# Optimization experiments

Measured on AMD Instinct MI355X. Metric: run time of the kernel, lower is better.

## Reference

```python
import jax, jax.numpy as jnp
import numpy as np

K = 9  # kernel_size (kNN neighbors, includes self since loop=True)


def _knn_edges(x_f, batch, k):
    # x_f: [N, C]. Full pairwise squared distances, masked across batch groups.
    N = x_f.shape[0]
    sq = jnp.sum(x_f * x_f, axis=1)
    d2 = sq[:, None] - 2.0 * (x_f @ x_f.T) + sq[None, :]          # [N, N]
    same = batch[:, None] == batch[None, :]
    d2 = jnp.where(same, d2, jnp.inf)
    neg_d, idx = jax.lax.top_k(-d2, k)                             # k nearest per query row
    valid = jnp.isfinite(neg_d)                                    # guard tiny groups (<k nodes)
    src = idx.reshape(-1)                                          # neighbor -> source
    tgt = jnp.repeat(jnp.arange(N), k)                             # query    -> target
    return src, tgt, valid.reshape(-1)


def _cheb_conv(x_f, src, tgt, valid, W0, W1, bias):
    # ChebConv, K=2, normalization='sym', lambda_max=2.0:
    #   out = x @ W0 + (L_hat x) @ W1 + b,  L_hat = -D^{-1/2} A D^{-1/2} (diag 0)
    N = x_f.shape[0]
    w = jnp.where(valid & (src != tgt), 1.0, 0.0)                  # remove_self_loops
    deg = jax.ops.segment_sum(w, src, num_segments=N)
    dis = jnp.where(deg > 0, jax.lax.rsqrt(jnp.maximum(deg, 1e-30)), 0.0)
    norm = -dis[src] * w * dis[tgt]                                # off-diag of scaled Laplacian
    Tx1 = jax.ops.segment_sum(norm[:, None] * x_f[src], tgt, num_segments=N)
    return x_f @ W0 + Tx1 @ W1 + bias


def setup_inputs() -> dict:
    key = jax.random.key(0)
    k1, k2, k3, k4 = jax.random.split(key, 4)
    B, C, H, W = 8, 192, 32, 32
    Cout = 192
    return {
        "x": jax.random.normal(k1, (B, C, H, W), dtype=jnp.float32),
        "W0": jax.random.normal(k2, (C, Cout), dtype=jnp.float32) * (1.0 / np.sqrt(C)),
        "W1": jax.random.normal(k3, (C, Cout), dtype=jnp.float32) * (1.0 / np.sqrt(C)),
        "bias": jax.random.normal(k4, (Cout,), dtype=jnp.float32) * 0.01,
    }


def reference(x, W0, W1, bias):
    B, C, H, W = x.shape
    N = B * H * W
    x_f = jnp.transpose(x, (0, 2, 3, 1)).reshape(N, C)             # flat_nodes: [B*H*W, C]
    # torch.linspace(0, B, steps=N, dtype=int64) -> truncated float linspace
    batch = jnp.linspace(0.0, float(B), N).astype(jnp.int32)
    src, tgt, valid = _knn_edges(x_f, batch, K)
    return _cheb_conv(x_f, src, tgt, valid, W0, W1, bias)
```

## Files before the change

### kernel.cpp

```cpp
#include <hip/hip_runtime.h>
#include <math.h>

#define NN 8192
#define CF 192
#define KNN 9
#define NSPL 8
#define PKS 12

typedef __bf16 v8bf __attribute__((ext_vector_type(8)));
typedef float f32x16 __attribute__((ext_vector_type(16)));
typedef float f32x4 __attribute__((ext_vector_type(4)));

__device__ __forceinline__ int group_start(int g) {
    int s = (8191 * g + 7) >> 3;
    return s > 8192 ? 8192 : s;
}

__device__ __forceinline__ float disf(int d) {
    return d > 0 ? 1.0f / sqrtf((float)d) : 0.0f;
}

__device__ __forceinline__ unsigned short f2bf(float f) {
    unsigned u = __float_as_uint(f);
    unsigned r = (u + 0x7FFFu + ((u >> 16) & 1u)) >> 16;
    return (unsigned short)r;
}
__device__ __forceinline__ float bf2f(unsigned short h) {
    return __uint_as_float(((unsigned)h) << 16);
}

__global__ __launch_bounds__(256) void transpose_kernel(
    const float* __restrict__ x, unsigned short* __restrict__ xh,
    unsigned short* __restrict__ xl, float* __restrict__ sq,
    int* __restrict__ deg)
{
    __shared__ float tile[32][65];
    int b = blockIdx.x, ht = blockIdx.y;
    int hw0 = ht * 64;
    int tid = threadIdx.x;
    if (tid < 64) deg[(b * 16 + ht) * 64 + tid] = 0;

    float sacc[8];
#pragma unroll
    for (int p = 0; p < 8; ++p) sacc[p] = 0.0f;

    for (int ct = 0; ct < 6; ++ct) {
        int c0 = ct * 32;
        __syncthreads();
#pragma unroll
        for (int p = 0; p < 8; ++p) {
            int c  = p * 4 + (tid >> 6);
            int hw = tid & 63;
            tile[c][hw] = x[(size_t)b * 196608 + (size_t)(c0 + c) * 1024 + hw0 + hw];
        }
        __syncthreads();
#pragma unroll
        for (int p = 0; p < 8; ++p) {
            int hw = p * 8 + (tid >> 5);
            int cc = tid & 31;
            float v = tile[cc][hw];
            size_t o = (size_t)(b * 1024 + hw0 + hw) * CF + c0 + cc;
            unsigned short h = f2bf(v);
            xh[o] = h;
            xl[o] = f2bf(v - bf2f(h));
            sacc[p] = fmaf(v, v, sacc[p]);
        }
    }
#pragma unroll
    for (int p = 0; p < 8; ++p) {
        float s = sacc[p];
#pragma unroll
        for (int off = 16; off > 0; off >>= 1) s += __shfl_xor(s, off, 32);
        if ((tid & 31) == 0)
            sq[(size_t)(b * 1024 + hw0 + p * 8 + (tid >> 5))] = s;
    }
}

__global__ __launch_bounds__(256, 2) void knn_kernel(
    const unsigned short* __restrict__ xh, const unsigned short* __restrict__ xl,
    const float* __restrict__ sq,
    float* __restrict__ pk_d, int* __restrict__ pk_i)
{
    int bid = blockIdx.x;
    int g = bid >> 7;
    int rem = bid & 127;
    int qb = rem >> 3;
    int split = rem & 7;
    int gs = group_start(g);
    int gsize = group_start(g + 1) - gs;
    int q0 = qb * 64;
    int nq = gsize - q0; if (nq > 64) nq = 64;
    if (nq <= 0) return;
    int c0 = split * 128;
    int ncc = gsize - c0; if (ncc > 128) ncc = 128;

    int tid = threadIdx.x;

    if (ncc <= 0) {
        if (tid < nq) {
            int q = gs + q0 + tid;
            size_t base = ((size_t)q * NSPL + split) * PKS;
#pragma unroll
            for (int j = 0; j < KNN; ++j) { pk_d[base + j] = __builtin_inff(); pk_i[base + j] = -1; }
        }
        return;
    }

    __shared__ __align__(16) char smem[28192];
    unsigned short (*Ah)[24] = (unsigned short(*)[24])smem;
    unsigned short (*Al)[24] = (unsigned short(*)[24])(smem + 3072);
    unsigned short (*Bh)[24] = (unsigned short(*)[24])(smem + 6144);
    unsigned short (*Bl)[24] = (unsigned short(*)[24])(smem + 12288);
    float (*ld)[KNN][65] = (float(*)[KNN][65])smem;
    int   (*li)[KNN][65] = (int(*)[KNN][65])(smem + 9360);
    float (*Ds)[37] = (float(*)[37])(smem + 18720);
    __shared__ float sqc_s[128];
    __shared__ float sqq_s[64];

    int lane = tid & 63, w = tid >> 6;
    int arow = (w & 1) * 32 + (lane & 31);
    int k8 = (lane >> 5) * 8;
    int brow0 = (w >> 1) * 64 + (lane & 31);

    if (tid < 64) {
        int qo = q0 + tid; if (qo > gsize - 1) qo = gsize - 1;
        sqq_s[tid] = sq[gs + qo];
    }
    if (tid < 128) {
        sqc_s[tid] = (tid < 128 && tid < ncc) ? sq[gs + c0 + tid] : __builtin_inff();
    }

    int a_hl = tid >> 7, a_r = (tid >> 1) & 63, a_half = tid & 1;
    int a_qo = q0 + a_r; if (a_qo > gsize - 1) a_qo = gsize - 1;
    const unsigned short* a_src = (a_hl ? xl : xh)
        + (size_t)(gs + a_qo) * CF + a_half * 8;
    unsigned short* a_dst = (a_hl ? (unsigned short*)Al : (unsigned short*)Ah)
        + a_r * 24 + a_half * 8;

    int b_r = (tid >> 1) & 127, b_half = tid & 1;
    int b_co = c0 + b_r; if (b_co > gsize - 1) b_co = gsize - 1;
    const unsigned short* b_src0 = xh + (size_t)(gs + b_co) * CF + b_half * 8;
    const unsigned short* b_src1 = xl + (size_t)(gs + b_co) * CF + b_half * 8;
    unsigned short* b_dst0 = (unsigned short*)Bh + b_r * 24 + b_half * 8;
    unsigned short* b_dst1 = (unsigned short*)Bl + b_r * 24 + b_half * 8;

    f32x16 acc[2];
#pragma unroll
    for (int t = 0; t < 2; ++t)
#pragma unroll
        for (int r = 0; r < 16; ++r) acc[t][r] = 0.0f;

    uint4 rA  = *(const uint4*)a_src;
    uint4 rB0 = *(const uint4*)b_src0;
    uint4 rB1 = *(const uint4*)b_src1;

    for (int kb = 0; kb < 12; ++kb) {
        __syncthreads();
        *(uint4*)a_dst  = rA;
        *(uint4*)b_dst0 = rB0;
        *(uint4*)b_dst1 = rB1;
        __syncthreads();
        if (kb < 11) {
            rA  = *(const uint4*)(a_src  + (kb + 1) * 16);
            rB0 = *(const uint4*)(b_src0 + (kb + 1) * 16);
            rB1 = *(const uint4*)(b_src1 + (kb + 1) * 16);
        }
        v8bf a_hi = *(const v8bf*)&Ah[arow][k8];
        v8bf a_lo = *(const v8bf*)&Al[arow][k8];
#pragma unroll
        for (int t = 0; t < 2; ++t) {
            v8bf b_hi = *(const v8bf*)&Bh[brow0 + t * 32][k8];
            v8bf b_lo = *(const v8bf*)&Bl[brow0 + t * 32][k8];
            acc[t] = __builtin_amdgcn_mfma_f32_32x32x16_bf16(a_hi, b_hi, acc[t], 0, 0, 0);
            acc[t] = __builtin_amdgcn_mfma_f32_32x32x16_bf16(a_lo, b_hi, acc[t], 0, 0, 0);
            acc[t] = __builtin_amdgcn_mfma_f32_32x32x16_bf16(a_hi, b_lo, acc[t], 0, 0, 0);
        }
    }

    int sq_ = tid & 63, sch = tid >> 6;
    float sqqv = sqq_s[sq_];
    float pd[KNN]; int pi[KNN];
#pragma unroll
    for (int j = 0; j < KNN; ++j) { pd[j] = __builtin_inff(); pi[j] = -1; }

#pragma unroll
    for (int qt = 0; qt < 4; ++qt) {
        __syncthreads();
        if ((w >> 1) == (qt >> 1)) {
#pragma unroll
            for (int r = 0; r < 16; ++r) {
                int row = (w & 1) * 32 + (r & 3) + 8 * (r >> 2) + 4 * (lane >> 5);
                Ds[row][lane & 31] = acc[qt & 1][r];
            }
        }
        __syncthreads();
        float dv[8], cv[8];
#pragma unroll
        for (int j8 = 0; j8 < 8; ++j8) {
            dv[j8] = Ds[sq_][sch * 8 + j8];
            cv[j8] = sqc_s[qt * 32 + sch * 8 + j8];
        }
#pragma unroll
        for (int j8 = 0; j8 < 8; ++j8) {
            float d = (sqqv - 2.0f * dv[j8]) + cv[j8];
            if (d < pd[KNN - 1]) {
                pd[KNN - 1] = d; pi[KNN - 1] = gs + c0 + qt * 32 + sch * 8 + j8;
#pragma unroll
                for (int j = KNN - 1; j > 0; --j) {
                    if (pd[j] < pd[j - 1]) {
                        float tf = pd[j]; pd[j] = pd[j - 1]; pd[j - 1] = tf;
                        int tn = pi[j]; pi[j] = pi[j - 1]; pi[j - 1] = tn;
                    }
                }
            }
        }
    }

#pragma unroll
    for (int j = 0; j < KNN; ++j) { ld[sch][j][sq_] = pd[j]; li[sch][j][sq_] = pi[j]; }
    __syncthreads();

    if (tid < 64) {
        float dL[4][KNN]; int iL[4][KNN];
#pragma unroll
        for (int ch = 0; ch < 4; ++ch)
#pragma unroll
            for (int j = 0; j < KNN; ++j) {
                dL[ch][j] = ld[ch][j][tid];
                iL[ch][j] = li[ch][j][tid];
            }
        float td[KNN]; int ti[KNN];
#pragma unroll
        for (int j = 0; j < KNN; ++j) { td[j] = __builtin_inff(); ti[j] = -1; }
#pragma unroll
        for (int ch = 0; ch < 4; ++ch) {
#pragma unroll
            for (int j0 = 0; j0 < KNN; ++j0) {
                float d = dL[ch][j0];
                if (!(d < td[KNN - 1])) break;
                td[KNN - 1] = d; ti[KNN - 1] = iL[ch][j0];
#pragma unroll
                for (int j = KNN - 1; j > 0; --j) {
                    if (td[j] < td[j - 1]) {
                        float tf = td[j]; td[j] = td[j - 1]; td[j - 1] = tf;
                        int tn = ti[j]; ti[j] = ti[j - 1]; ti[j - 1] = tn;
                    }
                }
            }
        }
        if (tid < nq) {
            int q = gs + q0 + tid;
            size_t base = ((size_t)q * NSPL + split) * PKS;
#pragma unroll
            for (int j = 0; j < KNN; ++j) { pk_d[base + j] = td[j]; pk_i[base + j] = ti[j]; }
        }
    }
}

__global__ __launch_bounds__(64) void merge_kernel(
    const float* __restrict__ pk_d, const int* __restrict__ pk_i,
    int* __restrict__ edges, int* __restrict__ deg,
    const float* __restrict__ W0, const float* __restrict__ W1,
    unsigned short* __restrict__ wt)
{
    __shared__ float wtile[32][33];
    int tid = threadIdx.x;
    if (blockIdx.x >= 128) {
        int wid = blockIdx.x - 128;
        int mat = wid / 36, rem2 = wid % 36;
        int k0 = (rem2 / 6) * 32, n0 = (rem2 % 6) * 32;
        const float* W = mat ? W1 : W0;
#pragma unroll
        for (int p = 0; p < 4; ++p) {
            int idx = p * 64 + tid;
            int k = idx >> 3, n4 = (idx & 7) * 4;
            *(float4*)&wtile[k][n4] =
                *(const float4*)(W + (size_t)(k0 + k) * CF + n0 + n4);
        }
        __syncthreads();
#pragma unroll
        for (int p = 0; p < 4; ++p) {
            int idx = p * 64 + tid;
            int n = idx >> 3, k4 = (idx & 7) * 4;
            ushort4 h;
            h.x = f2bf(wtile[k4 + 0][n]); h.y = f2bf(wtile[k4 + 1][n]);
            h.z = f2bf(wtile[k4 + 2][n]); h.w = f2bf(wtile[k4 + 3][n]);
            *(ushort4*)(wt + (size_t)mat * 36864 + (size_t)(n0 + n) * CF + k0 + k4) = h;
        }
        return;
    }
    int q = blockIdx.x * 64 + tid;
    float td[KNN]; int ti[KNN];
#pragma unroll
    for (int j = 0; j < KNN; ++j) { td[j] = __builtin_inff(); ti[j] = -1; }
#pragma unroll
    for (int sb = 0; sb < 2; ++sb) {
        float sd[4][KNN]; int si[4][KNN];
#pragma unroll
        for (int s2 = 0; s2 < 4; ++s2) {
            int s = sb * 4 + s2;
            const float* pd = pk_d + ((size_t)q * NSPL + s) * PKS;
            const int*   pp = pk_i + ((size_t)q * NSPL + s) * PKS;
            float4 d0 = *(const float4*)pd;
            float4 d1 = *(const float4*)(pd + 4);
            sd[s2][0] = d0.x; sd[s2][1] = d0.y; sd[s2][2] = d0.z; sd[s2][3] = d0.w;
            sd[s2][4] = d1.x; sd[s2][5] = d1.y; sd[s2][6] = d1.z; sd[s2][7] = d1.w;
            sd[s2][8] = pd[8];
            int4 i0 = *(const int4*)pp;
            int4 i1 = *(const int4*)(pp + 4);
            si[s2][0] = i0.x; si[s2][1] = i0.y; si[s2][2] = i0.z; si[s2][3] = i0.w;
            si[s2][4] = i1.x; si[s2][5] = i1.y; si[s2][6] = i1.z; si[s2][7] = i1.w;
            si[s2][8] = pp[8];
        }
#pragma unroll
        for (int s2 = 0; s2 < 4; ++s2) {
#pragma unroll
            for (int j0 = 0; j0 < KNN; ++j0) {
                float d = sd[s2][j0];
                if (!(d < td[KNN - 1])) break;
                td[KNN - 1] = d; ti[KNN - 1] = si[s2][j0];
#pragma unroll
                for (int j = KNN - 1; j > 0; --j) {
                    if (td[j] < td[j - 1]) {
                        float tf = td[j]; td[j] = td[j - 1]; td[j - 1] = tf;
                        int tn = ti[j]; ti[j] = ti[j - 1]; ti[j - 1] = tn;
                    }
                }
            }
        }
    }
#pragma unroll
    for (int j = 0; j < KNN; ++j) {
        int id = ti[j];
        edges[q * KNN + j] = id;
        if (id >= 0 && id != q) atomicAdd(&deg[id], 1);
    }
}

__global__ __launch_bounds__(256, 2) void out_kernel(
    const unsigned short* __restrict__ xh, const unsigned short* __restrict__ wt,
    const int* __restrict__ edges, const int* __restrict__ deg,
    const float* __restrict__ bias, float* __restrict__ out)
{
    __shared__ __align__(16) unsigned short A0s[16][200];
    __shared__ __align__(16) unsigned short A1s[16][200];
    __shared__ unsigned short Wts[2][CF][32];
    __shared__ float coef_s[16][KNN];
    __shared__ int   nb_s[16][KNN];

    int r0 = blockIdx.x * 16;
    int tid = threadIdx.x;

    for (int t = tid; t < 384; t += 256) {
        int i = t / 24, c8 = (t % 24) * 8;
        *(uint4*)&A0s[i][c8] = *(const uint4*)(xh + (size_t)(r0 + i) * CF + c8);
    }
    if (tid < 16 * KNN) {
        int i = tid / KNN, j = tid % KNN;
        int q = r0 + i;
        int id = edges[q * KNN + j];
        float cf = 0.0f; int s = q;
        if (id >= 0 && id != q) { cf = -disf(deg[id]) * disf(deg[q]); s = id; }
        coef_s[i][j] = cf; nb_s[i][j] = s;
    }
    __syncthreads();
    for (int e = tid; e < 16 * CF / 8; e += 256) {
        int i = e / 24, c8 = (e % 24) * 8;
        float a[8];
#pragma unroll
        for (int j = 0; j < 8; ++j) a[j] = 0.0f;
#pragma unroll
        for (int t = 0; t < KNN; ++t) {
            float cf = coef_s[i][t];
            uint4 v = *(const uint4*)(xh + (size_t)nb_s[i][t] * CF + c8);
            const unsigned short* pv = (const unsigned short*)&v;
#pragma unroll
            for (int j = 0; j < 8; ++j) a[j] = fmaf(cf, bf2f(pv[j]), a[j]);
        }
        uint4 hv;
        hv.x = (unsigned)f2bf(a[0]) | ((unsigned)f2bf(a[1]) << 16);
        hv.y = (unsigned)f2bf(a[2]) | ((unsigned)f2bf(a[3]) << 16);
        hv.z = (unsigned)f2bf(a[4]) | ((unsigned)f2bf(a[5]) << 16);
        hv.w = (unsigned)f2bf(a[6]) | ((unsigned)f2bf(a[7]) << 16);
        *(uint4*)&A1s[i][c8] = hv;
    }

    int lane = tid & 63, w = tid >> 6;
    int m = lane & 15;
    int kq = (lane >> 4) * 8;
    f32x4 acc[3];
#pragma unroll
    for (int t = 0; t < 3; ++t)
#pragma unroll
        for (int r = 0; r < 4; ++r) acc[t][r] = 0.0f;

    for (int kt = 0; kt < 6; ++kt) {
        __syncthreads();
#pragma unroll
        for (int p = 0; p < 6; ++p) {
            int f = p * 256 + tid;
            int mat = f / 768, n = (f % 768) / 4, k16 = (f % 4) * 8;
            *(uint4*)&Wts[mat][n][k16] =
                *(const uint4*)(wt + (size_t)mat * 36864 + (size_t)n * CF + kt * 32 + k16);
        }
        __syncthreads();
        v8bf a0 = *(const v8bf*)&A0s[m][kt * 32 + kq];
        v8bf a1 = *(const v8bf*)&A1s[m][kt * 32 + kq];
#pragma unroll
        for (int t3 = 0; t3 < 3; ++t3) {
            int n0 = w * 48 + t3 * 16;
            v8bf w0 = *(const v8bf*)&Wts[0][n0 + m][kq];
            v8bf w1 = *(const v8bf*)&Wts[1][n0 + m][kq];
            acc[t3] = __builtin_amdgcn_mfma_f32_16x16x32_bf16(a0, w0, acc[t3], 0, 0, 0);
            acc[t3] = __builtin_amdgcn_mfma_f32_16x16x32_bf16(a1, w1, acc[t3], 0, 0, 0);
        }
    }

    int col = lane & 15, rb = (lane >> 4) * 4;
#pragma unroll
    for (int t3 = 0; t3 < 3; ++t3) {
        int n0 = w * 48 + t3 * 16;
        float bv = bias[n0 + col];
#pragma unroll
        for (int r = 0; r < 4; ++r)
            out[(size_t)(r0 + rb + r) * CF + n0 + col] = acc[t3][r] + bv;
    }
}

extern "C" void kernel_launch(void* const* d_in, const int* in_sizes, int n_in,
                              void* d_out, int out_size, void* d_ws, size_t ws_size,
                              hipStream_t stream)
{
    const float* x    = (const float*)d_in[0];
    const float* W0   = (const float*)d_in[1];
    const float* W1   = (const float*)d_in[2];
    const float* bias = (const float*)d_in[3];
    float* out = (float*)d_out;

    char* ws = (char*)d_ws;
    unsigned short* xh = (unsigned short*)ws; ws += (size_t)NN * CF * 2;
    unsigned short* xl = (unsigned short*)ws; ws += (size_t)NN * CF * 2;
    float* sq    = (float*)ws;  ws += (size_t)NN * 4;
    int*   deg   = (int*)ws;    ws += (size_t)NN * 4;
    int*   edges = (int*)ws;    ws += (size_t)NN * KNN * 4;

    unsigned short* wt = xl;

    float* pk_d = out;
    int*   pk_i = (int*)(out + (size_t)NN * NSPL * PKS);

    hipLaunchKernelGGL(transpose_kernel, dim3(8, 16), dim3(256), 0, stream,
                       x, xh, xl, sq, deg);
    hipLaunchKernelGGL(knn_kernel, dim3(1152), dim3(256), 0, stream,
                       xh, xl, sq, pk_d, pk_i);
    hipLaunchKernelGGL(merge_kernel, dim3(200), dim3(64), 0, stream,
                       pk_d, pk_i, edges, deg, W0, W1, wt);
    hipLaunchKernelGGL(out_kernel, dim3(512), dim3(256), 0, stream,
                       xh, wt, edges, deg, bias, out);
}
```

Measured before the change: 131.5 us.

## Double-buffer LDS tiles in kNN distance and output GEMM kernels

The kNN distance kernel now double-buffers its A/B bf16 tiles in shared memory with a two-deep register prefetch, so each k-step needs one barrier instead of two. After the GEMM it writes the whole 64x128 distance tile to LDS at once instead of in four barrier-separated quarter passes. The output kernel double-buffers the weight tiles and prefetches them during the neighbor aggregation. The cost is more LDS and more registers per thread, which could reduce occupancy.

```diff
diff --git a/kernel.cpp b/kernel.cpp
--- a/kernel.cpp
+++ b/kernel.cpp
@@ -106,14 +106,8 @@
         return;
     }
 
-    __shared__ __align__(16) char smem[28192];
-    unsigned short (*Ah)[24] = (unsigned short(*)[24])smem;
-    unsigned short (*Al)[24] = (unsigned short(*)[24])(smem + 3072);
-    unsigned short (*Bh)[24] = (unsigned short(*)[24])(smem + 6144);
-    unsigned short (*Bl)[24] = (unsigned short(*)[24])(smem + 12288);
-    float (*ld)[KNN][65] = (float(*)[KNN][65])smem;
-    int   (*li)[KNN][65] = (int(*)[KNN][65])(smem + 9360);
-    float (*Ds)[37] = (float(*)[37])(smem + 18720);
+    __shared__ __align__(16) char smem[36864];
+    unsigned short* sm = (unsigned short*)smem;
     __shared__ float sqc_s[128];
     __shared__ float sqq_s[64];
 
@@ -127,22 +121,21 @@
         sqq_s[tid] = sq[gs + qo];
     }
     if (tid < 128) {
-        sqc_s[tid] = (tid < 128 && tid < ncc) ? sq[gs + c0 + tid] : __builtin_inff();
+        sqc_s[tid] = (tid < ncc) ? sq[gs + c0 + tid] : __builtin_inff();
     }
 
     int a_hl = tid >> 7, a_r = (tid >> 1) & 63, a_half = tid & 1;
     int a_qo = q0 + a_r; if (a_qo > gsize - 1) a_qo = gsize - 1;
     const unsigned short* a_src = (a_hl ? xl : xh)
         + (size_t)(gs + a_qo) * CF + a_half * 8;
-    unsigned short* a_dst = (a_hl ? (unsigned short*)Al : (unsigned short*)Ah)
-        + a_r * 24 + a_half * 8;
+    int a_off = a_hl * 1536 + a_r * 24 + a_half * 8;
 
     int b_r = (tid >> 1) & 127, b_half = tid & 1;
     int b_co = c0 + b_r; if (b_co > gsize - 1) b_co = gsize - 1;
     const unsigned short* b_src0 = xh + (size_t)(gs + b_co) * CF + b_half * 8;
     const unsigned short* b_src1 = xl + (size_t)(gs + b_co) * CF + b_half * 8;
-    unsigned short* b_dst0 = (unsigned short*)Bh + b_r * 24 + b_half * 8;
-    unsigned short* b_dst1 = (unsigned short*)Bl + b_r * 24 + b_half * 8;
+    int b_off0 = 3072 + b_r * 24 + b_half * 8;
+    int b_off1 = 6144 + b_r * 24 + b_half * 8;
 
     f32x16 acc[2];
 #pragma unroll
@@ -150,61 +143,77 @@
 #pragma unroll
         for (int r = 0; r < 16; ++r) acc[t][r] = 0.0f;
 
-    uint4 rA  = *(const uint4*)a_src;
-    uint4 rB0 = *(const uint4*)b_src0;
-    uint4 rB1 = *(const uint4*)b_src1;
-
+    uint4 sA[2], sB0[2], sB1[2];
+    sA[0]  = *(const uint4*)(a_src);       sA[1]  = *(const uint4*)(a_src + 16);
+    sB0[0] = *(const uint4*)(b_src0);      sB0[1] = *(const uint4*)(b_src0 + 16);
+    sB1[0] = *(const uint4*)(b_src1);      sB1[1] = *(const uint4*)(b_src1 + 16);
+    *(uint4*)(sm + a_off)  = sA[0];
+    *(uint4*)(sm + b_off0) = sB0[0];
+    *(uint4*)(sm + b_off1) = sB1[0];
+    sA[0]  = *(const uint4*)(a_src  + 32);
+    sB0[0] = *(const uint4*)(b_src0 + 32);
+    sB1[0] = *(const uint4*)(b_src1 + 32);
+    __syncthreads();
+
+#pragma unroll
     for (int kb = 0; kb < 12; ++kb) {
-        __syncthreads();
-        *(uint4*)a_dst  = rA;
-        *(uint4*)b_dst0 = rB0;
-        *(uint4*)b_dst1 = rB1;
-        __syncthreads();
+        const int cur = kb & 1, nxt = cur ^ 1;
         if (kb < 11) {
-            rA  = *(const uint4*)(a_src  + (kb + 1) * 16);
-            rB0 = *(const uint4*)(b_src0 + (kb + 1) * 16);
-            rB1 = *(const uint4*)(b_src1 + (kb + 1) * 16);
-        }
-        v8bf a_hi = *(const v8bf*)&Ah[arow][k8];
-        v8bf a_lo = *(const v8bf*)&Al[arow][k8];
+            *(uint4*)(sm + nxt * 9216 + a_off)  = sA[nxt];
+            *(uint4*)(sm + nxt * 9216 + b_off0) = sB0[nxt];
+            *(uint4*)(sm + nxt * 9216 + b_off1) = sB1[nxt];
+        }
+        if (kb < 9) {
+            sA[nxt]  = *(const uint4*)(a_src  + (kb + 3) * 16);
+            sB0[nxt] = *(const uint4*)(b_src0 + (kb + 3) * 16);
+            sB1[nxt] = *(const uint4*)(b_src1 + (kb + 3) * 16);
+        }
+        v8bf a_hi = *(const v8bf*)(sm + cur * 9216 + arow * 24 + k8);
+        v8bf a_lo = *(const v8bf*)(sm + cur * 9216 + 1536 + arow * 24 + k8);
 #pragma unroll
         for (int t = 0; t < 2; ++t) {
-            v8bf b_hi = *(const v8bf*)&Bh[brow0 + t * 32][k8];
-            v8bf b_lo = *(const v8bf*)&Bl[brow0 + t * 32][k8];
+            v8bf b_hi = *(const v8bf*)(sm + cur * 9216 + 3072 + (brow0 + t * 32) * 24 + k8);
+            v8bf b_lo = *(const v8bf*)(sm + cur * 9216 + 6144 + (brow0 + t * 32) * 24 + k8);
             acc[t] = __builtin_amdgcn_mfma_f32_32x32x16_bf16(a_hi, b_hi, acc[t], 0, 0, 0);
             acc[t] = __builtin_amdgcn_mfma_f32_32x32x16_bf16(a_lo, b_hi, acc[t], 0, 0, 0);
             acc[t] = __builtin_amdgcn_mfma_f32_32x32x16_bf16(a_hi, b_lo, acc[t], 0, 0, 0);
         }
-    }
+        __syncthreads();
+    }
+
+    float (*Ds)[133] = (float(*)[133])smem;
+#pragma unroll
+    for (int t = 0; t < 2; ++t)
+#pragma unroll
+        for (int r = 0; r < 16; ++r) {
+            int row = (w & 1) * 32 + (r & 3) + 8 * (r >> 2) + 4 * (lane >> 5);
+            int col = (w >> 1) * 64 + t * 32 + (lane & 31);
+            Ds[row][col] = acc[t][r];
+        }
+    __syncthreads();
 
     int sq_ = tid & 63, sch = tid >> 6;
     float sqqv = sqq_s[sq_];
+    float dv[32], cvv[32];
+#pragma unroll
+    for (int qt = 0; qt < 4; ++qt)
+#pragma unroll
+        for (int j8 = 0; j8 < 8; ++j8) {
+            int c = qt * 32 + sch * 8 + j8;
+            dv[qt * 8 + j8] = Ds[sq_][c];
+            cvv[qt * 8 + j8] = sqc_s[c];
+        }
     float pd[KNN]; int pi[KNN];
 #pragma unroll
     for (int j = 0; j < KNN; ++j) { pd[j] = __builtin_inff(); pi[j] = -1; }
-
-#pragma unroll
-    for (int qt = 0; qt < 4; ++qt) {
-        __syncthreads();
-        if ((w >> 1) == (qt >> 1)) {
-#pragma unroll
-            for (int r = 0; r < 16; ++r) {
-                int row = (w & 1) * 32 + (r & 3) + 8 * (r >> 2) + 4 * (lane >> 5);
-                Ds[row][lane & 31] = acc[qt & 1][r];
-            }
-        }
-        __syncthreads();
-        float dv[8], cv[8];
+#pragma unroll
+    for (int qt = 0; qt < 4; ++qt)
 #pragma unroll
         for (int j8 = 0; j8 < 8; ++j8) {
-            dv[j8] = Ds[sq_][sch * 8 + j8];
-            cv[j8] = sqc_s[qt * 32 + sch * 8 + j8];
-        }
-#pragma unroll
-        for (int j8 = 0; j8 < 8; ++j8) {
-            float d = (sqqv - 2.0f * dv[j8]) + cv[j8];
+            int c = qt * 32 + sch * 8 + j8;
+            float d = (sqqv - 2.0f * dv[qt * 8 + j8]) + cvv[qt * 8 + j8];
             if (d < pd[KNN - 1]) {
-                pd[KNN - 1] = d; pi[KNN - 1] = gs + c0 + qt * 32 + sch * 8 + j8;
+                pd[KNN - 1] = d; pi[KNN - 1] = gs + c0 + c;
 #pragma unroll
                 for (int j = KNN - 1; j > 0; --j) {
                     if (pd[j] < pd[j - 1]) {
@@ -214,8 +223,10 @@
                 }
             }
         }
-    }
-
+    __syncthreads();
+
+    float (*ld)[KNN][65] = (float(*)[KNN][65])smem;
+    int   (*li)[KNN][65] = (int(*)[KNN][65])(smem + 9360);
 #pragma unroll
     for (int j = 0; j < KNN; ++j) { ld[sch][j][sq_] = pd[j]; li[sch][j][sq_] = pi[j]; }
     __syncthreads();
@@ -344,12 +355,31 @@
 {
     __shared__ __align__(16) unsigned short A0s[16][200];
     __shared__ __align__(16) unsigned short A1s[16][200];
-    __shared__ unsigned short Wts[2][CF][32];
+    __shared__ unsigned short Wts[2][2][CF][32];
     __shared__ float coef_s[16][KNN];
     __shared__ int   nb_s[16][KNN];
 
     int r0 = blockIdx.x * 16;
     int tid = threadIdx.x;
+
+#define LDW(dst, kt_)                                                          \
+    _Pragma("unroll")                                                          \
+    for (int p = 0; p < 6; ++p) {                                              \
+        int f = p * 256 + tid;                                                 \
+        int mat = f / 768, n = (f % 768) / 4, k16 = (f % 4) * 8;               \
+        dst[p] = *(const uint4*)(wt + (size_t)mat * 36864 + (size_t)n * CF     \
+                                 + (kt_) * 32 + k16);                          \
+    }
+#define STW(buf_, src)                                                         \
+    _Pragma("unroll")                                                          \
+    for (int p = 0; p < 6; ++p) {                                              \
+        int f = p * 256 + tid;                                                 \
+        int mat = f / 768, n = (f % 768) / 4, k16 = (f % 4) * 8;               \
+        *(uint4*)&Wts[buf_][mat][n][k16] = src[p];                             \
+    }
+
+    uint4 wr[2][6];
+    LDW(wr[0], 0);
 
     for (int t = tid; t < 384; t += 256) {
         int i = t / 24, c8 = (t % 24) * 8;
@@ -363,6 +393,7 @@
         if (id >= 0 && id != q) { cf = -disf(deg[id]) * disf(deg[q]); s = id; }
         coef_s[i][j] = cf; nb_s[i][j] = s;
     }
+    LDW(wr[1], 1);
     __syncthreads();
     for (int e = tid; e < 16 * CF / 8; e += 256) {
         int i = e / 24, c8 = (e % 24) * 8;
@@ -384,6 +415,9 @@
         hv.w = (unsigned)f2bf(a[6]) | ((unsigned)f2bf(a[7]) << 16);
         *(uint4*)&A1s[i][c8] = hv;
     }
+    STW(0, wr[0]);
+    LDW(wr[0], 2);
+    __syncthreads();
 
     int lane = tid & 63, w = tid >> 6;
     int m = lane & 15;
@@ -394,26 +428,22 @@
 #pragma unroll
         for (int r = 0; r < 4; ++r) acc[t][r] = 0.0f;
 
+#pragma unroll
     for (int kt = 0; kt < 6; ++kt) {
-        __syncthreads();
-#pragma unroll
-        for (int p = 0; p < 6; ++p) {
-            int f = p * 256 + tid;
-            int mat = f / 768, n = (f % 768) / 4, k16 = (f % 4) * 8;
-            *(uint4*)&Wts[mat][n][k16] =
-                *(const uint4*)(wt + (size_t)mat * 36864 + (size_t)n * CF + kt * 32 + k16);
-        }
-        __syncthreads();
+        const int cur = kt & 1, nxt = cur ^ 1;
+        if (kt < 5) { STW(nxt, wr[nxt]); }
+        if (kt < 3) { LDW(wr[nxt], kt + 3); }
         v8bf a0 = *(const v8bf*)&A0s[m][kt * 32 + kq];
         v8bf a1 = *(const v8bf*)&A1s[m][kt * 32 + kq];
 #pragma unroll
         for (int t3 = 0; t3 < 3; ++t3) {
             int n0 = w * 48 + t3 * 16;
-            v8bf w0 = *(const v8bf*)&Wts[0][n0 + m][kq];
-            v8bf w1 = *(const v8bf*)&Wts[1][n0 + m][kq];
+            v8bf w0 = *(const v8bf*)&Wts[cur][0][n0 + m][kq];
+            v8bf w1 = *(const v8bf*)&Wts[cur][1][n0 + m][kq];
             acc[t3] = __builtin_amdgcn_mfma_f32_16x16x32_bf16(a0, w0, acc[t3], 0, 0, 0);
             acc[t3] = __builtin_amdgcn_mfma_f32_16x16x32_bf16(a1, w1, acc[t3], 0, 0, 0);
         }
+        __syncthreads();
     }
 
     int col = lane & 15, rb = (lane >> 4) * 4;
@@ -425,6 +455,8 @@
         for (int r = 0; r < 4; ++r)
             out[(size_t)(r0 + rb + r) * CF + n0 + col] = acc[t3][r] + bv;
     }
+#undef LDW
+#undef STW
 }
 
 extern "C" void kernel_launch(void* const* d_in, const int* in_sizes, int n_in,
```

Measured after the change: 172.5 us. 31.1% more time.

## Widen GEMM k-step to 32, cut barriers, stage whole distance tile once

Applied to the files above, without the earlier changes.

The bf16-split distance GEMM now loads 32-wide K slices, six iterations instead of twelve, with each thread moving six 16-byte chunks and a padded 40-element LDS row stride. This halves the main-loop barrier count. The full 64x128 accumulator tile is written to shared memory once, which replaces four staged round trips with their paired barriers. Shared memory per block grows, which may lower occupancy, and the hi/lo pointers are now derived from xh plus an NN*CF offset, so the code assumes xl sits right after xh.

```diff
diff --git a/kernel.cpp b/kernel.cpp
--- a/kernel.cpp
+++ b/kernel.cpp
@@ -106,14 +106,8 @@
         return;
     }
 
-    __shared__ __align__(16) char smem[28192];
-    unsigned short (*Ah)[24] = (unsigned short(*)[24])smem;
-    unsigned short (*Al)[24] = (unsigned short(*)[24])(smem + 3072);
-    unsigned short (*Bh)[24] = (unsigned short(*)[24])(smem + 6144);
-    unsigned short (*Bl)[24] = (unsigned short(*)[24])(smem + 12288);
-    float (*ld)[KNN][65] = (float(*)[KNN][65])smem;
-    int   (*li)[KNN][65] = (int(*)[KNN][65])(smem + 9360);
-    float (*Ds)[37] = (float(*)[37])(smem + 18720);
+    __shared__ __align__(16) char smem[34048];
+    unsigned short* sm = (unsigned short*)smem;
     __shared__ float sqc_s[128];
     __shared__ float sqq_s[64];
 
@@ -127,22 +121,25 @@
         sqq_s[tid] = sq[gs + qo];
     }
     if (tid < 128) {
-        sqc_s[tid] = (tid < 128 && tid < ncc) ? sq[gs + c0 + tid] : __builtin_inff();
-    }
-
-    int a_hl = tid >> 7, a_r = (tid >> 1) & 63, a_half = tid & 1;
-    int a_qo = q0 + a_r; if (a_qo > gsize - 1) a_qo = gsize - 1;
-    const unsigned short* a_src = (a_hl ? xl : xh)
-        + (size_t)(gs + a_qo) * CF + a_half * 8;
-    unsigned short* a_dst = (a_hl ? (unsigned short*)Al : (unsigned short*)Ah)
-        + a_r * 24 + a_half * 8;
-
-    int b_r = (tid >> 1) & 127, b_half = tid & 1;
-    int b_co = c0 + b_r; if (b_co > gsize - 1) b_co = gsize - 1;
-    const unsigned short* b_src0 = xh + (size_t)(gs + b_co) * CF + b_half * 8;
-    const unsigned short* b_src1 = xl + (size_t)(gs + b_co) * CF + b_half * 8;
-    unsigned short* b_dst0 = (unsigned short*)Bh + b_r * 24 + b_half * 8;
-    unsigned short* b_dst1 = (unsigned short*)Bl + b_r * 24 + b_half * 8;
+        sqc_s[tid] = (tid < ncc) ? sq[gs + c0 + tid] : __builtin_inff();
+    }
+
+    int rr = tid >> 2, q4 = tid & 3;
+    int aq = q0 + rr; if (aq > gsize - 1) aq = gsize - 1;
+    int cqA = c0 + rr;      if (cqA > gsize - 1) cqA = gsize - 1;
+    int cqB = c0 + 64 + rr; if (cqB > gsize - 1) cqB = gsize - 1;
+    int g0 = (gs + aq)  * CF + q4 * 8;
+    int g1 = g0 + NN * CF;
+    int g2 = (gs + cqA) * CF + q4 * 8;
+    int g3 = (gs + cqB) * CF + q4 * 8;
+    int g4 = g2 + NN * CF;
+    int g5 = g3 + NN * CF;
+    int s0 = rr * 40 + q4 * 8;
+    int s1 = s0 + 2560;
+    int s2 = 5120 + s0;
+    int s3 = s2 + 2560;
+    int s4 = s2 + 5120;
+    int s5 = s3 + 5120;
 
     f32x16 acc[2];
 #pragma unroll
@@ -150,55 +147,64 @@
 #pragma unroll
         for (int r = 0; r < 16; ++r) acc[t][r] = 0.0f;
 
-    uint4 rA  = *(const uint4*)a_src;
-    uint4 rB0 = *(const uint4*)b_src0;
-    uint4 rB1 = *(const uint4*)b_src1;
-
-    for (int kb = 0; kb < 12; ++kb) {
-        __syncthreads();
-        *(uint4*)a_dst  = rA;
-        *(uint4*)b_dst0 = rB0;
-        *(uint4*)b_dst1 = rB1;
-        __syncthreads();
-        if (kb < 11) {
-            rA  = *(const uint4*)(a_src  + (kb + 1) * 16);
-            rB0 = *(const uint4*)(b_src0 + (kb + 1) * 16);
-            rB1 = *(const uint4*)(b_src1 + (kb + 1) * 16);
-        }
-        v8bf a_hi = *(const v8bf*)&Ah[arow][k8];
-        v8bf a_lo = *(const v8bf*)&Al[arow][k8];
-#pragma unroll
-        for (int t = 0; t < 2; ++t) {
-            v8bf b_hi = *(const v8bf*)&Bh[brow0 + t * 32][k8];
-            v8bf b_lo = *(const v8bf*)&Bl[brow0 + t * 32][k8];
-            acc[t] = __builtin_amdgcn_mfma_f32_32x32x16_bf16(a_hi, b_hi, acc[t], 0, 0, 0);
-            acc[t] = __builtin_amdgcn_mfma_f32_32x32x16_bf16(a_lo, b_hi, acc[t], 0, 0, 0);
-            acc[t] = __builtin_amdgcn_mfma_f32_32x32x16_bf16(a_hi, b_lo, acc[t], 0, 0, 0);
-        }
-    }
+    uint4 d0, d1, d2, d3, d4, d5;
+    d0 = *(const uint4*)(xh + g0); d1 = *(const uint4*)(xh + g1);
+    d2 = *(const uint4*)(xh + g2); d3 = *(const uint4*)(xh + g3);
+    d4 = *(const uint4*)(xh + g4); d5 = *(const uint4*)(xh + g5);
+
+    for (int kb = 0; kb < 6; ++kb) {
+        *(uint4*)(sm + s0) = d0; *(uint4*)(sm + s1) = d1;
+        *(uint4*)(sm + s2) = d2; *(uint4*)(sm + s3) = d3;
+        *(uint4*)(sm + s4) = d4; *(uint4*)(sm + s5) = d5;
+        __syncthreads();
+        if (kb < 5) {
+            int o = (kb + 1) * 32;
+            d0 = *(const uint4*)(xh + g0 + o); d1 = *(const uint4*)(xh + g1 + o);
+            d2 = *(const uint4*)(xh + g2 + o); d3 = *(const uint4*)(xh + g3 + o);
+            d4 = *(const uint4*)(xh + g4 + o); d5 = *(const uint4*)(xh + g5 + o);
+        }
+#pragma unroll
+        for (int h = 0; h < 2; ++h) {
+            int ao = arow * 40 + h * 16 + k8;
+            v8bf a_hi = *(const v8bf*)(sm + ao);
+            v8bf a_lo = *(const v8bf*)(sm + 2560 + ao);
+#pragma unroll
+            for (int t = 0; t < 2; ++t) {
+                int bo = 5120 + (brow0 + t * 32) * 40 + h * 16 + k8;
+                v8bf b_hi = *(const v8bf*)(sm + bo);
+                v8bf b_lo = *(const v8bf*)(sm + 5120 + bo);
+                acc[t] = __builtin_amdgcn_mfma_f32_32x32x16_bf16(a_hi, b_hi, acc[t], 0, 0, 0);
+                acc[t] = __builtin_amdgcn_mfma_f32_32x32x16_bf16(a_lo, b_hi, acc[t], 0, 0, 0);
+                acc[t] = __builtin_amdgcn_mfma_f32_32x32x16_bf16(a_hi, b_lo, acc[t], 0, 0, 0);
+            }
+        }
+        __syncthreads();
+    }
+
+    float (*Ds)[133] = (float(*)[133])smem;
+#pragma unroll
+    for (int t = 0; t < 2; ++t)
+#pragma unroll
+        for (int r = 0; r < 16; ++r) {
+            int row = (w & 1) * 32 + (r & 3) + 8 * (r >> 2) + 4 * (lane >> 5);
+            int col = (w >> 1) * 64 + t * 32 + (lane & 31);
+            Ds[row][col] = acc[t][r];
+        }
+    __syncthreads();
 
     int sq_ = tid & 63, sch = tid >> 6;
     float sqqv = sqq_s[sq_];
     float pd[KNN]; int pi[KNN];
 #pragma unroll
     for (int j = 0; j < KNN; ++j) { pd[j] = __builtin_inff(); pi[j] = -1; }
-
 #pragma unroll
     for (int qt = 0; qt < 4; ++qt) {
-        __syncthreads();
-        if ((w >> 1) == (qt >> 1)) {
-#pragma unroll
-            for (int r = 0; r < 16; ++r) {
-                int row = (w & 1) * 32 + (r & 3) + 8 * (r >> 2) + 4 * (lane >> 5);
-                Ds[row][lane & 31] = acc[qt & 1][r];
-            }
-        }
-        __syncthreads();
         float dv[8], cv[8];
 #pragma unroll
         for (int j8 = 0; j8 < 8; ++j8) {
-            dv[j8] = Ds[sq_][sch * 8 + j8];
-            cv[j8] = sqc_s[qt * 32 + sch * 8 + j8];
+            int c = qt * 32 + sch * 8 + j8;
+            dv[j8] = Ds[sq_][c];
+            cv[j8] = sqc_s[c];
         }
 #pragma unroll
         for (int j8 = 0; j8 < 8; ++j8) {
@@ -215,7 +221,10 @@
             }
         }
     }
-
+    __syncthreads();
+
+    float (*ld)[KNN][65] = (float(*)[KNN][65])smem;
+    int   (*li)[KNN][65] = (int(*)[KNN][65])(smem + 9360);
 #pragma unroll
     for (int j = 0; j < KNN; ++j) { ld[sch][j][sq_] = pd[j]; li[sch][j][sq_] = pi[j]; }
     __syncthreads();
```

Result: faster. 121.7 us (-7.5%).
